# Optimization experiments

Hardware: AMD Instinct MI355X
Metric: run time of the kernel (lower is better)

## Reference

```python
import math
import jax, jax.numpy as jnp
import numpy as np

B = 1024
D = 384
Q = 65536
TOPK = 128
HARD_W = 2.0
TEMP_START = 0.2
TEMP_END = 0.05
WARMUP = 10


def _temperature(epoch):
    # curriculum cosine decay (epoch is a Python int)
    if epoch >= WARMUP:
        return TEMP_END
    progress = epoch / max(1, WARMUP)
    return TEMP_END + 0.5 * (TEMP_START - TEMP_END) * (1.0 + math.cos(math.pi * progress))


def _normalize(x):
    # F.normalize: x / max(||x||, eps)
    n = jnp.linalg.norm(x, axis=-1, keepdims=True)
    return x / jnp.maximum(n, 1e-12)


def _hard_neg_reweight(logits):
    # logits: [B, N]; labels = arange(B) (diagonal positives)
    b = logits.shape[0]
    rows = jnp.arange(b)
    neg_logits = logits.at[rows, rows].set(-jnp.inf)      # mask positives
    _, hard_idx = jax.lax.top_k(neg_logits, TOPK)          # [B, TOPK] hardest negatives
    weights = jnp.ones_like(logits)
    weights = weights.at[rows[:, None], hard_idx].set(HARD_W)
    weights = weights.at[rows, rows].set(1.0)
    return logits * weights


def _cross_entropy_diag(logits):
    b = logits.shape[0]
    logp = jax.nn.log_softmax(logits, axis=-1)
    return -jnp.mean(logp[jnp.arange(b), jnp.arange(b)])


def setup_inputs() -> dict:
    key = jax.random.key(0)
    k1, k2, k3, k4 = jax.random.split(key, 4)
    rgb_feat = jax.random.normal(k1, (B, D), dtype=jnp.float32)
    ir_feat = jax.random.normal(k2, (B, D), dtype=jnp.float32)
    rgb_queue = _normalize(jax.random.normal(k3, (Q, D), dtype=jnp.float32))
    ir_queue = _normalize(jax.random.normal(k4, (Q, D), dtype=jnp.float32))
    return {"rgb_feat": rgb_feat, "ir_feat": ir_feat,
            "rgb_queue": rgb_queue, "ir_queue": ir_queue, "epoch": 0}


def reference(rgb_feat, ir_feat, rgb_queue, ir_queue, epoch):
    temp = _temperature(epoch)
    rgb_z = _normalize(rgb_feat.astype(jnp.float32))
    ir_z = _normalize(ir_feat.astype(jnp.float32))
    ir_all = jnp.concatenate([ir_z, ir_queue], axis=0)    # [B+Q, D]
    rgb_all = jnp.concatenate([rgb_z, rgb_queue], axis=0)
    logits_r2i = (rgb_z @ ir_all.T) / temp                # [B, B+Q]
    logits_i2r = (ir_z @ rgb_all.T) / temp
    logits_r2i = _hard_neg_reweight(logits_r2i)
    logits_i2r = _hard_neg_reweight(logits_i2r)
    return 0.5 * (_cross_entropy_diag(logits_r2i) + _cross_entropy_diag(logits_i2r))
```

## Files before the change

### kernel.cpp

```cpp
#include <hip/hip_runtime.h>
#include <hip/hip_bf16.h>

#define B_    1024
#define D_    384
#define Q_    65536
#define N_    66560
#define TOPK_ 128

#define NBIN_ 4096
#define CAP_  2048
#define SRANK_ 24
#define SLOTS_ 17

typedef __bf16 bf16x8 __attribute__((ext_vector_type(8)));
typedef float  f32x4  __attribute__((ext_vector_type(4)));
typedef unsigned short u16;
typedef u16 u16x8 __attribute__((ext_vector_type(8)));

__device__ __forceinline__ unsigned short f2bf(float x) {
  unsigned int u = __float_as_uint(x);
  unsigned int r = (u + 0x7fffu + ((u >> 16) & 1u)) >> 16;
  return (unsigned short)r;
}

__device__ __forceinline__ void gld_lds16(const void* g, void* l) {
  __builtin_amdgcn_global_load_lds(
      (__attribute__((address_space(1))) void*)(g),
      (__attribute__((address_space(3))) void*)(l), 16, 0, 0);
}

__device__ __forceinline__ void wait_vmcnt(int n) {
  switch (n) {
    case 4:  asm volatile("s_waitcnt vmcnt(4)"  ::: "memory"); break;
    default: asm volatile("s_waitcnt vmcnt(0)"  ::: "memory"); break;
  }
}

__device__ __forceinline__ unsigned int bf2key(unsigned int u) {
  return u ^ ((u & 0x8000u) ? 0xFFFFu : 0x8000u);
}
__device__ __forceinline__ float key2val(unsigned int k) {
  unsigned int u = (k & 0x8000u) ? (k ^ 0x8000u) : (~k & 0xFFFFu);
  return __uint_as_float(u << 16);
}

__global__ __launch_bounds__(64) void k_normalize(
    const float* __restrict__ rgb, const float* __restrict__ ir,
    const int* __restrict__ ep,
    u16* __restrict__ zrA, u16* __restrict__ ziA,
    u16* __restrict__ zrU, u16* __restrict__ ziU)
{
  int r = blockIdx.x & (B_ - 1);
  bool isIr = blockIdx.x >= B_;
  const float* src = (isIr ? ir : rgb) + (size_t)r * D_;
  u16* dA = (isIr ? ziA : zrA) + (size_t)r * D_;
  u16* dU = (isIr ? ziU : zrU) + (size_t)r * D_;
  int t = threadIdx.x;
  float x[6]; float ss = 0.f;
  #pragma unroll
  for (int k = 0; k < 6; ++k) { x[k] = src[t + 64*k]; ss += x[k]*x[k]; }
  #pragma unroll
  for (int off = 32; off > 0; off >>= 1) ss += __shfl_down(ss, off);
  ss = __shfl(ss, 0);
  float inv = 1.0f / fmaxf(sqrtf(ss), 1e-12f);

  int e = ep[0];
  float temp;
  if (e >= 10) temp = 0.05f;
  else {
    float p = (float)e * 0.1f;
    temp = 0.05f + 0.075f * (1.0f + cosf(3.14159265358979323846f * p));
  }
  float itemp = 1.0f / temp;

  #pragma unroll
  for (int k = 0; k < 6; ++k) {
    float z = x[k] * inv;
    dU[t + 64*k] = f2bf(z);
    dA[t + 64*k] = f2bf(z * itemp);
  }
}

__global__ __launch_bounds__(256) void k_build_ball(
    const u16* __restrict__ zU, const float* __restrict__ queue,
    u16* __restrict__ ball)
{
  size_t i = ((size_t)blockIdx.x * 256 + threadIdx.x) * 8;
  const size_t zElems = (size_t)B_ * D_;
  if (i < zElems) {
    *(uint4*)(ball + i) = *(const uint4*)(zU + i);
  } else {
    const float* q = queue + (i - zElems);
    float4 a = *(const float4*)q;
    float4 b = *(const float4*)(q + 4);
    u16x8 o;
    o[0] = f2bf(a.x); o[1] = f2bf(a.y); o[2] = f2bf(a.z); o[3] = f2bf(a.w);
    o[4] = f2bf(b.x); o[5] = f2bf(b.y); o[6] = f2bf(b.z); o[7] = f2bf(b.w);
    *(u16x8*)(ball + i) = o;
  }
}

#define BK_ 32
#define NSTEP_ 12
__global__ __launch_bounds__(256, 3) void k_gemm(
    const u16* __restrict__ A,
    const u16* __restrict__ ball,
    u16* __restrict__ C,
    float* __restrict__ diag,
    int r0, int mtiles)
{
  __shared__ __align__(16) unsigned char smem[49152];
  u16* Ct = (u16*)smem;

  int bid = blockIdx.x;
  int nwg = gridDim.x;
  int cpx = nwg >> 3;
  int wgid = (bid & 7) * cpx + (bid >> 3);
  int nt = wgid / mtiles;
  int mt = wgid - nt * mtiles;

  const int tid  = threadIdx.x;
  const int wave = tid >> 6, lane = tid & 63;
  const int wm = wave >> 1, wn = wave & 1;
  const int mbase = mt * 128;
  const int nbase = nt * 128;
  const u16* Ab = A    + (size_t)(r0 + mbase) * D_;
  const u16* Bb = ball + (size_t)nbase * D_;

  auto As = [&](int t) -> u16* { return (u16*)(smem + (t % 3) * 16384); };
  auto Bs = [&](int t) -> u16* { return (u16*)(smem + (t % 3) * 16384 + 8192); };
  auto stage = [&](int t) {
    const int ks = t * BK_;
    #pragma unroll
    for (int i = 0; i < 2; ++i) {
      int f = i * 256 + tid;
      int rr = f >> 2, cc = f & 3;
      int koff = (((cc * 16) ^ (((rr >> 1) & 3) << 4)) >> 1);
      gld_lds16(Ab + (size_t)rr * D_ + ks + koff, As(t) + (size_t)f * 8);
      gld_lds16(Bb + (size_t)rr * D_ + ks + koff, Bs(t) + (size_t)f * 8);
    }
  };

  f32x4 acc[4][4];
  #pragma unroll
  for (int m = 0; m < 4; ++m)
    #pragma unroll
    for (int n = 0; n < 4; ++n)
      #pragma unroll
      for (int r = 0; r < 4; ++r) acc[m][n][r] = 0.0f;

  const int lr = lane & 15;
  const int kb = (lane >> 4) * 16;

  stage(0); stage(1);

  #pragma unroll
  for (int t = 0; t < NSTEP_; ++t) {
    wait_vmcnt(t < NSTEP_ - 1 ? 4 : 0);
    __builtin_amdgcn_s_barrier();
    __builtin_amdgcn_sched_barrier(0);

    const u16* Ac = As(t);
    const u16* Bc = Bs(t);
    bf16x8 af[4], bq[4];
    #pragma unroll
    for (int m = 0; m < 4; ++m) {
      int row = wm*64 + m*16 + lr;
      af[m] = *(const bf16x8*)((const char*)Ac + row * 64 + (kb ^ (((row >> 1) & 3) << 4)));
    }
    #pragma unroll
    for (int n = 0; n < 4; ++n) {
      int row = wn*64 + n*16 + lr;
      bq[n] = *(const bf16x8*)((const char*)Bc + row * 64 + (kb ^ (((row >> 1) & 3) << 4)));
    }
    if (t + 2 < NSTEP_) stage(t + 2);

    #pragma unroll
    for (int m = 0; m < 4; ++m)
      #pragma unroll
      for (int n = 0; n < 4; ++n)
        acc[m][n] = __builtin_amdgcn_mfma_f32_16x16x32_bf16(af[m], bq[n], acc[m][n], 0, 0, 0);

    asm volatile("s_waitcnt lgkmcnt(0)" ::: "memory");
    __builtin_amdgcn_sched_barrier(0);
  }
  __syncthreads();

  const int rowq = (lane >> 4) * 4;
  #pragma unroll
  for (int m = 0; m < 4; ++m) {
    #pragma unroll
    for (int n = 0; n < 4; ++n) {
      int lcol = wn*64 + n*16 + lr;
      int gcol = nbase + lcol;
      #pragma unroll
      for (int r = 0; r < 4; ++r) {
        int lrow = wm*64 + m*16 + rowq + r;
        float x = acc[m][n][r];
        int grow = r0 + mbase + lrow;
        if (gcol == grow) { diag[grow] = x; x = -60.0f; }
        Ct[lrow * 136 + lcol] = f2bf(x);
      }
    }
  }
  __syncthreads();

  int rrow = tid >> 4;
  int cchunk = (tid & 15) * 8;
  #pragma unroll
  for (int pass = 0; pass < 8; ++pass) {
    int row = pass * 16 + rrow;
    u16x8 v = *(const u16x8*)(Ct + row * 136 + cchunk);
    *(u16x8*)(C + (size_t)(mbase + row) * N_ + nbase + cchunk) = v;
  }
}

__global__ __launch_bounds__(256) void k_select(
    const u16* __restrict__ C, const float* __restrict__ diag,
    float* __restrict__ rowloss, int r0)
{
  __shared__ unsigned int hist[NBIN_];
  __shared__ u16 keyslots[256 * SLOTS_];
  __shared__ float vals[CAP_];
  __shared__ float fred[256];
  __shared__ unsigned int csum[256];
  __shared__ int lcnt[256];
  __shared__ unsigned int subhist[16];
  __shared__ float sh_d2;
  __shared__ int shv[4];

  const int t = threadIdx.x;
  const int grow = r0 + blockIdx.x;
  const u16x8* p = (const u16x8*)(C + (size_t)blockIdx.x * N_);

  uint4* h4 = (uint4*)hist;
  #pragma unroll
  for (int i = 0; i < 4; ++i) h4[i * 256 + t] = make_uint4(0,0,0,0);
  if (t < 16) subhist[t] = 0;
  if (t == 0) { shv[2] = 0; sh_d2 = 0.f; }
  __syncthreads();

  {
    u16x8 s0 = p[t * 32];
    u16x8 s1 = p[t * 32 + 16];
    #pragma unroll
    for (int e = 0; e < 8; ++e) {
      atomicAdd(&hist[bf2key((unsigned int)(unsigned short)s0[e]) >> 4], 1u);
      atomicAdd(&hist[bf2key((unsigned int)(unsigned short)s1[e]) >> 4], 1u);
    }
  }
  __syncthreads();
  {
    unsigned int S = 0;
    #pragma unroll
    for (int i = 0; i < 16; ++i) S += hist[t * 16 + i];
    csum[t] = S;
    __syncthreads();
    unsigned int a = S;
    #pragma unroll
    for (int s = 1; s < 256; s <<= 1) {
      unsigned int add = (t + s < 256) ? csum[t + s] : 0u;
      __syncthreads();
      a += add; csum[t] = a;
      __syncthreads();
    }
    int above = (t < 255) ? (int)csum[t + 1] : 0;
    if (above < SRANK_ && above + (int)S >= SRANK_) {
      int cum = above;
      #pragma unroll 1
      for (int i = 15; i >= 0; --i) {
        int c = (int)hist[t * 16 + i];
        if (cum + c >= SRANK_) { shv[3] = t * 16 + i; break; }
        cum += c;
      }
    }
  }
  __syncthreads();
  const unsigned int tfine = (unsigned int)shv[3];
  #pragma unroll
  for (int i = 0; i < 4; ++i) h4[i * 256 + t] = make_uint4(0,0,0,0);
  __syncthreads();

  u16* myslots = keyslots + t * SLOTS_;
  int lc = 0;
  float es0 = 0.f, es1 = 0.f;
  #pragma unroll 1
  for (int base = 0; base < 8192; base += 2048) {
    u16x8 v[8];
    #pragma unroll
    for (int j = 0; j < 8; ++j) v[j] = p[base + j * 256 + t];
    #pragma unroll
    for (int j = 0; j < 8; ++j) {
      #pragma unroll
      for (int e = 0; e < 8; ++e) {
        unsigned int u = (unsigned int)(unsigned short)v[j][e];
        unsigned int k = bf2key(u);
        float ex = __expf(__uint_as_float(u << 16));
        if (j & 1) es1 += ex; else es0 += ex;
        myslots[lc < 16 ? lc : 16] = (u16)k;
        lc += ((k >> 4) >= tfine);
      }
    }
  }
  if (t < 128) {
    u16x8 v = p[8192 + t];
    #pragma unroll
    for (int e = 0; e < 8; ++e) {
      unsigned int u = (unsigned int)(unsigned short)v[e];
      unsigned int k = bf2key(u);
      es0 += __expf(__uint_as_float(u << 16));
      myslots[lc < 16 ? lc : 16] = (u16)k;
      lc += ((k >> 4) >= tfine);
    }
  }
  float esum = es0 + es1;
  lcnt[t] = lc;
  __syncthreads();

  {
    unsigned int a = (unsigned int)lcnt[t];
    csum[t] = a;
    __syncthreads();
    #pragma unroll
    for (int s = 128; s > 0; s >>= 1) {
      unsigned int add = (t < s) ? csum[t + s] : 0u;
      __syncthreads();
      if (t < s) csum[t] = csum[t] + add;
      __syncthreads();
    }
  }
  const int cntTot = (int)csum[0];
  int ok_lc = __syncthreads_and(lc <= 16);

  float delta = 0.f;
  if (ok_lc && cntTot >= TOPK_) {
    #pragma unroll 1
    for (int i = t; i < 256 * 16; i += 256) {
      int ts = i >> 4, sl = i & 15;
      int c = lcnt[ts]; c = c < 16 ? c : 16;
      if (sl < c)
        atomicAdd(&hist[(unsigned int)keyslots[ts * SLOTS_ + sl] >> 4], 1u);
    }
    __syncthreads();
    unsigned int S = 0;
    #pragma unroll
    for (int i = 0; i < 16; ++i) S += hist[t * 16 + i];
    csum[t] = S;
    __syncthreads();
    unsigned int a = S;
    #pragma unroll
    for (int s = 1; s < 256; s <<= 1) {
      unsigned int add = (t + s < 256) ? csum[t + s] : 0u;
      __syncthreads();
      a += add; csum[t] = a;
      __syncthreads();
    }
    int above_chunk = (t < 255) ? (int)csum[t + 1] : 0;
    if (above_chunk < TOPK_ && above_chunk + (int)S >= TOPK_) {
      int cum = above_chunk;
      #pragma unroll 1
      for (int i = 15; i >= 0; --i) {
        int c = (int)hist[t * 16 + i];
        if (cum + c >= TOPK_) { shv[0] = t * 16 + i; shv[1] = cum; break; }
        cum += c;
      }
    }
    __syncthreads();
    const unsigned int bstar = (unsigned int)shv[0];
    const int need0 = TOPK_ - shv[1];
    #pragma unroll 1
    for (int i = t; i < 256 * 16; i += 256) {
      int ts = i >> 4, sl = i & 15;
      int c = lcnt[ts]; c = c < 16 ? c : 16;
      if (sl < c) {
        unsigned int k = (unsigned int)keyslots[ts * SLOTS_ + sl];
        unsigned int bin = k >> 4;
        if (bin > bstar) {
          float v = key2val(k);
          delta += __expf(2.f * v) - __expf(v);
        } else if (bin == bstar) {
          atomicAdd(&subhist[k & 15], 1u);
        }
      }
    }
    __syncthreads();
    if (t == 0) {
      int need = need0; float d2 = 0.f;
      #pragma unroll 1
      for (int sk = 15; sk >= 0 && need > 0; --sk) {
        int c = (int)subhist[sk];
        if (c > 0) {
          int take = c < need ? c : need;
          float v = key2val((bstar << 4) | (unsigned int)sk);
          d2 += (float)take * (__expf(2.f * v) - __expf(v));
          need -= take;
        }
      }
      sh_d2 = d2;
    }
  } else {
    #pragma unroll 1
    for (int base = 0; base < 8192; base += 2048) {
      u16x8 v[8];
      #pragma unroll
      for (int j = 0; j < 8; ++j) v[j] = p[base + j * 256 + t];
      #pragma unroll
      for (int j = 0; j < 8; ++j)
        #pragma unroll
        for (int e = 0; e < 8; ++e)
          atomicAdd(&hist[bf2key((unsigned int)(unsigned short)v[j][e]) >> 4], 1u);
    }
    if (t < 128) {
      u16x8 v = p[8192 + t];
      #pragma unroll
      for (int e = 0; e < 8; ++e)
        atomicAdd(&hist[bf2key((unsigned int)(unsigned short)v[e]) >> 4], 1u);
    }
    __syncthreads();
    unsigned int S = 0;
    #pragma unroll
    for (int i = 0; i < 16; ++i) S += hist[t * 16 + i];
    csum[t] = S;
    __syncthreads();
    unsigned int a = S;
    #pragma unroll
    for (int s = 1; s < 256; s <<= 1) {
      unsigned int add = (t + s < 256) ? csum[t + s] : 0u;
      __syncthreads();
      a += add; csum[t] = a;
      __syncthreads();
    }
    int above_chunk = (t < 255) ? (int)csum[t + 1] : 0;
    if (above_chunk < TOPK_ && above_chunk + (int)S >= TOPK_) {
      int cum = above_chunk;
      #pragma unroll 1
      for (int i = 15; i >= 0; --i) {
        int c = (int)hist[t * 16 + i];
        if (cum + c >= TOPK_) { shv[0] = t * 16 + i; shv[1] = cum; break; }
        cum += c;
      }
    }
    __syncthreads();
    const unsigned int bstar = (unsigned int)shv[0];
    const int need0 = TOPK_ - shv[1];
    #pragma unroll 1
    for (int base = 0; base < 8192; base += 2048) {
      u16x8 v[8];
      #pragma unroll
      for (int j = 0; j < 8; ++j) v[j] = p[base + j * 256 + t];
      #pragma unroll
      for (int j = 0; j < 8; ++j) {
        #pragma unroll
        for (int e = 0; e < 8; ++e) {
          unsigned int u = (unsigned int)(unsigned short)v[j][e];
          unsigned int bin = bf2key(u) >> 4;
          if (bin >= bstar) {
            float val = __uint_as_float(u << 16);
            if (bin > bstar) delta += __expf(2.f * val) - __expf(val);
            else { int s = atomicAdd(&shv[2], 1); if (s < CAP_) vals[s] = val; }
          }
        }
      }
    }
    if (t < 128) {
      u16x8 v = p[8192 + t];
      #pragma unroll
      for (int e = 0; e < 8; ++e) {
        unsigned int u = (unsigned int)(unsigned short)v[e];
        unsigned int bin = bf2key(u) >> 4;
        if (bin >= bstar) {
          float val = __uint_as_float(u << 16);
          if (bin > bstar) delta += __expf(2.f * val) - __expf(val);
          else { int s = atomicAdd(&shv[2], 1); if (s < CAP_) vals[s] = val; }
        }
      }
    }
    __syncthreads();
    int C2 = shv[2] < CAP_ ? shv[2] : CAP_;
    for (int i = t; i < C2; i += 256) {
      float v = vals[i];
      int g = 0;
      for (int k = 0; k < C2; ++k)
        g += (vals[k] > v) || (vals[k] == v && k < i);
      if (g < need0) delta += __expf(2.f * v) - __expf(v);
    }
  }

  fred[t] = esum + delta;
  __syncthreads();
  #pragma unroll
  for (int s = 128; s > 0; s >>= 1) { if (t < s) fred[t] += fred[t + s]; __syncthreads(); }

  if (t == 0) {
    float d = diag[grow];
    rowloss[grow] = logf(fred[0] + sh_d2 + __expf(d)) - d;
  }
}

__global__ __launch_bounds__(256) void k_final(
    const float* __restrict__ rowloss, float* __restrict__ out)
{
  __shared__ float red[256];
  int t = threadIdx.x;
  float s = 0.f;
  for (int i = t; i < 2 * B_; i += 256) s += rowloss[i];
  red[t] = s;
  __syncthreads();
  for (int k = 128; k > 0; k >>= 1) { if (t < k) red[t] += red[t + k]; __syncthreads(); }
  if (t == 0) out[0] = red[0] * (1.0f / (2.0f * B_));
}

extern "C" void kernel_launch(void* const* d_in, const int* in_sizes, int n_in,
                              void* d_out, int out_size, void* d_ws, size_t ws_size,
                              hipStream_t stream)
{
  const float* rgb_feat = (const float*)d_in[0];
  const float* ir_feat  = (const float*)d_in[1];
  const float* rgb_q    = (const float*)d_in[2];
  const float* ir_q     = (const float*)d_in[3];
  const int*   epoch    = (const int*)d_in[4];

  char* ws = (char*)d_ws;
  size_t off = 0;
  auto alloc = [&](size_t bytes) -> char* {
    char* p = ws + off;
    off = (off + bytes + 255) & ~(size_t)255;
    return p;
  };

  u16* zrA = (u16*)alloc((size_t)B_ * D_ * 2);
  u16* ziA = (u16*)alloc((size_t)B_ * D_ * 2);
  u16* zrU = (u16*)alloc((size_t)B_ * D_ * 2);
  u16* ziU = (u16*)alloc((size_t)B_ * D_ * 2);
  float* diag    = (float*)alloc((size_t)2 * B_ * 4);
  float* rowloss = (float*)alloc((size_t)2 * B_ * 4);
  u16* ball = (u16*)alloc((size_t)N_ * D_ * 2);

  size_t avail = ws_size > off ? ws_size - off : 0;
  int SR = (int)(avail / ((size_t)N_ * 2));
  SR &= ~127;
  if (SR > B_) SR = B_;
  if (SR < 128) SR = 128;
  u16* slab = (u16*)(ws + off);

  k_normalize<<<dim3(2 * B_), dim3(64), 0, stream>>>(
      rgb_feat, ir_feat, epoch, zrA, ziA, zrU, ziU);

  for (int dir = 0; dir < 2; ++dir) {
    const u16*   Amat   = (dir == 0) ? zrA : ziA;
    const u16*   zOther = (dir == 0) ? ziU : zrU;
    const float* queue  = (dir == 0) ? ir_q : rgb_q;
    float* diagD = diag    + dir * B_;
    float* lossD = rowloss + dir * B_;

    k_build_ball<<<dim3((unsigned)((size_t)N_ * D_ / 8 / 256)), dim3(256), 0, stream>>>(
        zOther, queue, ball);

    for (int r0 = 0; r0 < B_; r0 += SR) {
      int cur = (B_ - r0) < SR ? (B_ - r0) : SR;
      int mtiles = cur / 128;
      int nwg = (N_ / 128) * mtiles;
      k_gemm<<<dim3(nwg), dim3(256), 0, stream>>>(
          Amat, ball, slab, diagD, r0, mtiles);
      k_select<<<dim3(cur), dim3(256), 0, stream>>>(slab, diagD, lossD, r0);
    }
  }

  k_final<<<dim3(1), dim3(256), 0, stream>>>(rowloss, (float*)d_out);
}
```

Before: 298.8 us.

## Overlap second-direction ball build with first select in one fused launch

When the workspace holds the full 1024-row slab, the second direction's bf16 ball build is merged into the first direction's select kernel as extra blocks in a combined grid, so the memory-bound conversion overlaps with the selection work. Select shared memory moves to one packed buffer with `vals` aliased onto `keyslots`, and launch bounds now allow 5 blocks per CU for more occupancy. The fast path only applies when SR equals B; otherwise the original per-direction loop is kept. The risk is contention between the two kinds of block and a dependence on the workspace size.

Measured after the change: 329.3 us. +10.2%, slower.

```diff
diff --git a/kernel.cpp b/kernel.cpp
--- a/kernel.cpp
+++ b/kernel.cpp
@@ -11,6 +11,16 @@
 #define CAP_  2048
 #define SRANK_ 24
 #define SLOTS_ 17
+#define NBALLC_ 12480
+
+#define SM_HIST_   0
+#define SM_KEYS_   16384
+#define SM_FRED_   (16384 + 8704)
+#define SM_CSUM_   (SM_FRED_ + 1024)
+#define SM_LCNT_   (SM_CSUM_ + 1024)
+#define SM_SUBH_   (SM_LCNT_ + 1024)
+#define SM_SHV_    (SM_SUBH_ + 64)
+#define SM_SIZE_   (SM_SHV_ + 64)
 
 typedef __bf16 bf16x8 __attribute__((ext_vector_type(8)));
 typedef float  f32x4  __attribute__((ext_vector_type(4)));
@@ -81,11 +91,11 @@
   }
 }
 
-__global__ __launch_bounds__(256) void k_build_ball(
-    const u16* __restrict__ zU, const float* __restrict__ queue,
-    u16* __restrict__ ball)
-{
-  size_t i = ((size_t)blockIdx.x * 256 + threadIdx.x) * 8;
+__device__ __forceinline__ void ball_body(
+    int idx, int tid, const u16* __restrict__ zU,
+    const float* __restrict__ queue, u16* __restrict__ ball)
+{
+  size_t i = ((size_t)idx * 256 + tid) * 8;
   const size_t zElems = (size_t)B_ * D_;
   if (i < zElems) {
     *(uint4*)(ball + i) = *(const uint4*)(zU + i);
@@ -100,6 +110,13 @@
   }
 }
 
+__global__ __launch_bounds__(256) void k_build_ball(
+    const u16* __restrict__ zU, const float* __restrict__ queue,
+    u16* __restrict__ ball)
+{
+  ball_body(blockIdx.x, threadIdx.x, zU, queue, ball);
+}
+
 #define BK_ 32
 #define NSTEP_ 12
 __global__ __launch_bounds__(256, 3) void k_gemm(
@@ -215,29 +232,30 @@
   }
 }
 
-__global__ __launch_bounds__(256) void k_select(
+__device__ void select_body(
+    char* smem, int sbid,
     const u16* __restrict__ C, const float* __restrict__ diag,
     float* __restrict__ rowloss, int r0)
 {
-  __shared__ unsigned int hist[NBIN_];
-  __shared__ u16 keyslots[256 * SLOTS_];
-  __shared__ float vals[CAP_];
-  __shared__ float fred[256];
-  __shared__ unsigned int csum[256];
-  __shared__ int lcnt[256];
-  __shared__ unsigned int subhist[16];
-  __shared__ float sh_d2;
-  __shared__ int shv[4];
+  unsigned int* hist   = (unsigned int*)(smem + SM_HIST_);
+  u16*        keyslots = (u16*)(smem + SM_KEYS_);
+  float*      vals     = (float*)(smem + SM_KEYS_);
+  float*      fred     = (float*)(smem + SM_FRED_);
+  unsigned int* csum   = (unsigned int*)(smem + SM_CSUM_);
+  int*        lcnt     = (int*)(smem + SM_LCNT_);
+  unsigned int* subhist= (unsigned int*)(smem + SM_SUBH_);
+  int*        shv      = (int*)(smem + SM_SHV_);
+  float*      sh_d2    = (float*)(smem + SM_SHV_ + 16);
 
   const int t = threadIdx.x;
-  const int grow = r0 + blockIdx.x;
-  const u16x8* p = (const u16x8*)(C + (size_t)blockIdx.x * N_);
+  const int grow = r0 + sbid;
+  const u16x8* p = (const u16x8*)(C + (size_t)sbid * N_);
 
   uint4* h4 = (uint4*)hist;
   #pragma unroll
   for (int i = 0; i < 4; ++i) h4[i * 256 + t] = make_uint4(0,0,0,0);
   if (t < 16) subhist[t] = 0;
-  if (t == 0) { shv[2] = 0; sh_d2 = 0.f; }
+  if (t == 0) { shv[2] = 0; sh_d2[0] = 0.f; }
   __syncthreads();
 
   {
@@ -318,8 +336,7 @@
   __syncthreads();
 
   {
-    unsigned int a = (unsigned int)lcnt[t];
-    csum[t] = a;
+    csum[t] = (unsigned int)lcnt[t];
     __syncthreads();
     #pragma unroll
     for (int s = 128; s > 0; s >>= 1) {
@@ -396,7 +413,7 @@
           need -= take;
         }
       }
-      sh_d2 = d2;
+      sh_d2[0] = d2;
     }
   } else {
     #pragma unroll 1
@@ -493,8 +510,31 @@
 
   if (t == 0) {
     float d = diag[grow];
-    rowloss[grow] = logf(fred[0] + sh_d2 + __expf(d)) - d;
-  }
+    rowloss[grow] = logf(fred[0] + sh_d2[0] + __expf(d)) - d;
+  }
+}
+
+__global__ __launch_bounds__(256, 5) void k_select(
+    const u16* __restrict__ C, const float* __restrict__ diag,
+    float* __restrict__ rowloss, int r0)
+{
+  __shared__ __align__(16) char smem[SM_SIZE_];
+  select_body(smem, blockIdx.x, C, diag, rowloss, r0);
+}
+
+__global__ __launch_bounds__(256, 5) void k_selball(
+    const u16* sC, const float* sDiag, float* sRow, int s_r0, int s_nblk,
+    const u16* bZ, const float* bQ, u16* bBall, int b_nblk)
+{
+  __shared__ __align__(16) char smem[SM_SIZE_];
+  int bid = blockIdx.x;
+  if (bid < s_nblk) {
+    select_body(smem, bid, sC, sDiag, sRow, s_r0);
+    return;
+  }
+  int b0 = bid - s_nblk;
+  for (int idx = b0; idx < NBALLC_; idx += b_nblk)
+    ball_body(idx, threadIdx.x, bZ, bQ, bBall);
 }
 
 __global__ __launch_bounds__(256) void k_final(
@@ -546,23 +586,35 @@
   k_normalize<<<dim3(2 * B_), dim3(64), 0, stream>>>(
       rgb_feat, ir_feat, epoch, zrA, ziA, zrU, ziU);
 
-  for (int dir = 0; dir < 2; ++dir) {
-    const u16*   Amat   = (dir == 0) ? zrA : ziA;
-    const u16*   zOther = (dir == 0) ? ziU : zrU;
-    const float* queue  = (dir == 0) ? ir_q : rgb_q;
-    float* diagD = diag    + dir * B_;
-    float* lossD = rowloss + dir * B_;
-
-    k_build_ball<<<dim3((unsigned)((size_t)N_ * D_ / 8 / 256)), dim3(256), 0, stream>>>(
-        zOther, queue, ball);
-
-    for (int r0 = 0; r0 < B_; r0 += SR) {
-      int cur = (B_ - r0) < SR ? (B_ - r0) : SR;
-      int mtiles = cur / 128;
-      int nwg = (N_ / 128) * mtiles;
-      k_gemm<<<dim3(nwg), dim3(256), 0, stream>>>(
-          Amat, ball, slab, diagD, r0, mtiles);
-      k_select<<<dim3(cur), dim3(256), 0, stream>>>(slab, diagD, lossD, r0);
+  if (SR == B_) {
+    k_build_ball<<<dim3(NBALLC_), dim3(256), 0, stream>>>(ziU, ir_q, ball);
+    k_gemm<<<dim3((N_ / 128) * (B_ / 128)), dim3(256), 0, stream>>>(
+        zrA, ball, slab, diag, 0, B_ / 128);
+    k_selball<<<dim3(1024 + 2048), dim3(256), 0, stream>>>(
+        slab, diag, rowloss, 0, 1024,
+        zrU, rgb_q, ball, 2048);
+    k_gemm<<<dim3((N_ / 128) * (B_ / 128)), dim3(256), 0, stream>>>(
+        ziA, ball, slab, diag + B_, 0, B_ / 128);
+    k_select<<<dim3(1024), dim3(256), 0, stream>>>(
+        slab, diag + B_, rowloss + B_, 0);
+  } else {
+    for (int dir = 0; dir < 2; ++dir) {
+      const u16*   Amat   = (dir == 0) ? zrA : ziA;
+      const u16*   zOther = (dir == 0) ? ziU : zrU;
+      const float* queue  = (dir == 0) ? ir_q : rgb_q;
+      float* diagD = diag    + dir * B_;
+      float* lossD = rowloss + dir * B_;
+
+      k_build_ball<<<dim3(NBALLC_), dim3(256), 0, stream>>>(zOther, queue, ball);
+
+      for (int r0 = 0; r0 < B_; r0 += SR) {
+        int cur = (B_ - r0) < SR ? (B_ - r0) : SR;
+        int mtiles = cur / 128;
+        int nwg = (N_ / 128) * mtiles;
+        k_gemm<<<dim3(nwg), dim3(256), 0, stream>>>(
+            Amat, ball, slab, diagD, r0, mtiles);
+        k_select<<<dim3(cur), dim3(256), 0, stream>>>(slab, diagD, lossD, r0);
+      }
     }
   }
 
```
